# Kernel optimization log

Hardware: AMD Instinct MI355X
Metric: run time of the kernel (lower is better)

Reference implementation:

```python
import jax, jax.numpy as jnp
import numpy as np

L, S, N, E, H = 1024, 1024, 8, 1024, 16

def setup_inputs() -> dict:
    key = jax.random.key(0)
    k0, k1, k2, k3 = jax.random.split(key, 4)
    query = jax.random.normal(k0, (L, N, E), jnp.float32)
    key_t = jax.random.normal(k1, (S, N, E), jnp.float32)
    in_proj_weight = jax.random.normal(k2, (3 * E, E), jnp.float32) * (1.0 / np.sqrt(E))
    in_proj_bias = jnp.zeros((3 * E,), jnp.float32)
    attn_bias = jax.random.normal(k3, (N * H, L, S), jnp.float32) * 0.02
    return {"query": query, "key": key_t, "in_proj_weight": in_proj_weight,
            "in_proj_bias": in_proj_bias, "attn_bias": attn_bias}

def reference(query, key, in_proj_weight, in_proj_bias, attn_bias):
    tgt_len, bsz, embed_dim = query.shape
    head_dim = embed_dim // H
    scaling = float(head_dim) ** -0.5  # scale_factor = 1
    # q/k projections: first two embed_dim-row slices of in_proj_weight
    q = query @ in_proj_weight[:embed_dim].T + in_proj_bias[:embed_dim]
    k = key @ in_proj_weight[embed_dim:2 * embed_dim].T + in_proj_bias[embed_dim:2 * embed_dim]
    q = q * scaling
    # (L, N, E) -> (N*H, L, hd)
    q = q.reshape(tgt_len, bsz * H, head_dim).transpose(1, 0, 2)
    k = k.reshape(-1, bsz * H, head_dim).transpose(1, 0, 2)
    # scores: (N*H, L, S), additive bias, then stable softmax
    scores = jnp.einsum('bld,bsd->bls', q, k) + attn_bias
    attn_output_weights = jax.nn.softmax(scores, axis=-1)
    return attn_output_weights
```

## Files before the change

kernel.cpp:

```cpp
#include <hip/hip_runtime.h>
#include <hip/hip_bf16.h>
#include <stdint.h>

#define L_DIM 1024
#define S_DIM 1024
#define N_DIM 8
#define E_DIM 1024
#define H_DIM 16
#define HD    64
#define BH    (N_DIM*H_DIM)
#define M_ROWS (L_DIM*N_DIM)

typedef __bf16 bf16x8 __attribute__((ext_vector_type(8)));
typedef float  f32x4  __attribute__((ext_vector_type(4)));
typedef _Float16 f16;
typedef _Float16 f16x8 __attribute__((ext_vector_type(8)));
typedef unsigned short u16;
typedef unsigned short u16x8 __attribute__((ext_vector_type(8)));

__device__ inline u16 f2bf(float x){
  unsigned int u = __float_as_uint(x);
  u = (u + 0x7FFFu + ((u >> 16) & 1u)) >> 16;
  return (u16)u;
}

__global__ __launch_bounds__(256) void convert_kernel(
    const float* __restrict__ query, const float* __restrict__ key,
    const float* __restrict__ w,
    u16* __restrict__ qbf, u16* __restrict__ kbf,
    u16* __restrict__ wq, u16* __restrict__ wk)
{
  const int QN = M_ROWS*E_DIM;
  const int WN = E_DIM*E_DIM;
  const int total8 = (2*QN + 2*WN)/8;
  int stride = gridDim.x*blockDim.x;
  for (int g = blockIdx.x*blockDim.x + threadIdx.x; g < total8; g += stride) {
    int base = g*8;
    const float* src; u16* dst; float scale = 1.0f;
    if (base < QN)           { src = query + base;      dst = qbf + base; }
    else if (base < 2*QN)    { src = key + (base-QN);   dst = kbf + (base-QN); }
    else if (base < 2*QN+WN) { src = w + (base-2*QN);   dst = wq + (base-2*QN); scale = 0.125f; }
    else                     { src = w + (base-2*QN);   dst = wk + (base-2*QN-WN); }
    float4 v0 = *(const float4*)(src);
    float4 v1 = *(const float4*)(src+4);
    u16x8 o;
    o[0]=f2bf(v0.x*scale); o[1]=f2bf(v0.y*scale); o[2]=f2bf(v0.z*scale); o[3]=f2bf(v0.w*scale);
    o[4]=f2bf(v1.x*scale); o[5]=f2bf(v1.y*scale); o[6]=f2bf(v1.z*scale); o[7]=f2bf(v1.w*scale);
    *(u16x8*)dst = o;
  }
}

__global__ __launch_bounds__(256) void proj_gemm(
    const u16* __restrict__ A, const u16* __restrict__ W,
    const float* __restrict__ bias, float bscale,
    u16* __restrict__ C)
{
  __shared__ __align__(16) u16 As[128*32];
  __shared__ __align__(16) u16 Bs[128*32];
  const int t = threadIdx.x;
  const int lane = t & 63;
  const int w = t >> 6;
  const int wr = w >> 1, wc = w & 1;
  const int rowTile = blockIdx.x * 128;
  const int colTile = blockIdx.y * 128;

  f32x4 acc[4][4];
  #pragma unroll
  for (int m=0;m<4;m++)
    #pragma unroll
    for (int n=0;n<4;n++) acc[m][n] = (f32x4){0.f,0.f,0.f,0.f};

  uint32_t asBase = (uint32_t)(uintptr_t)&As[0];
  uint32_t bsBase = (uint32_t)(uintptr_t)&Bs[0];
  const char* Ab = (const char*)A;
  const char* Wb = (const char*)W;

  for (int kt = 0; kt < 32; ++kt) {
    __syncthreads();
    #pragma unroll
    for (int issue = 0; issue < 2; ++issue) {
      int o = issue*4096 + t*16;
      int row  = o >> 6;
      int colb = o & 63;
      const char* ga = Ab + (size_t)(rowTile + row)*2048 + kt*64 + colb;
      const char* gb = Wb + (size_t)(colTile + row)*2048 + kt*64 + colb;
      uint32_t la = asBase + issue*4096 + (w<<10);
      uint32_t lb = bsBase + issue*4096 + (w<<10);
      __builtin_amdgcn_global_load_lds(
          (const __attribute__((address_space(1))) void*)(uintptr_t)ga,
          (__attribute__((address_space(3))) void*)(uintptr_t)la, 16, 0, 0);
      __builtin_amdgcn_global_load_lds(
          (const __attribute__((address_space(1))) void*)(uintptr_t)gb,
          (__attribute__((address_space(3))) void*)(uintptr_t)lb, 16, 0, 0);
    }
    __syncthreads();

    bf16x8 af[4], bfr[4];
    int krow = (lane >> 4) * 16;
    #pragma unroll
    for (int m=0;m<4;m++) {
      int r = wr*64 + m*16 + (lane&15);
      af[m] = *(const bf16x8*)((const char*)As + r*64 + krow);
    }
    #pragma unroll
    for (int n=0;n<4;n++) {
      int r = wc*64 + n*16 + (lane&15);
      bfr[n] = *(const bf16x8*)((const char*)Bs + r*64 + krow);
    }
    #pragma unroll
    for (int m=0;m<4;m++)
      #pragma unroll
      for (int n=0;n<4;n++)
        acc[m][n] = __builtin_amdgcn_mfma_f32_16x16x32_bf16(af[m], bfr[n], acc[m][n], 0,0,0);
  }

  #pragma unroll
  for (int n=0;n<4;n++) {
    int gcol = colTile + wc*64 + n*16 + (lane&15);
    float bv = bias[gcol]*bscale;
    #pragma unroll
    for (int m=0;m<4;m++) {
      int grow0 = rowTile + wr*64 + m*16 + ((lane>>4)<<2);
      #pragma unroll
      for (int r=0;r<4;r++)
        C[(size_t)(grow0+r)*1024 + gcol] = f2bf(acc[m][n][r] + bv);
    }
  }
}

__global__ __launch_bounds__(256) void attn_softmax(
    const u16* __restrict__ Qb, const u16* __restrict__ Kb,
    const float* __restrict__ bias, float* __restrict__ out)
{
  __shared__ __align__(16) char scb[16*2048];
  const int t = threadIdx.x;
  const int lane = t & 63;
  const int w = t >> 6;
  const int ltile = blockIdx.x;
  const int b = blockIdx.y;
  const int n = b >> 4, h = b & 15;

  int l_row = ltile*16 + (lane & 15);
  size_t qoff = ((size_t)(l_row*8 + n))*1024 + h*64 + ((lane>>4)*8);
  bf16x8 a0 = *(const bf16x8*)(Qb + qoff);
  bf16x8 a1 = *(const bf16x8*)(Qb + qoff + 32);

  const int rowBase = (lane>>4)*4;

  for (int st = w; st < 64; st += 4) {
    int s_row = st*16 + (lane & 15);
    size_t koff = ((size_t)(s_row*8 + n))*1024 + h*64 + ((lane>>4)*8);
    bf16x8 b0 = *(const bf16x8*)(Kb + koff);
    bf16x8 b1 = *(const bf16x8*)(Kb + koff + 32);
    f32x4 acc = {0.f,0.f,0.f,0.f};
    acc = __builtin_amdgcn_mfma_f32_16x16x32_bf16(a0, b0, acc, 0,0,0);
    acc = __builtin_amdgcn_mfma_f32_16x16x32_bf16(a1, b1, acc, 0,0,0);
    int scol = st*16 + (lane & 15);
    #pragma unroll
    for (int r=0;r<4;r++) {
      int row = rowBase + r;
      int byte = (row*2048 + scol*2) ^ ((row&7)<<4);
      *(f16*)(scb + byte) = (f16)acc[r];
    }
  }
  __syncthreads();

  #pragma unroll
  for (int rr=0;rr<4;rr++) {
    int row = rr*4 + w;
    int l_glob = ltile*16 + row;
    const float* brow = bias + ((size_t)b*1024 + l_glob)*1024;
    float*       orow = out  + ((size_t)b*1024 + l_glob)*1024;
    const int swz = (row&7)<<4;
    float v[16];
    float mx = -1e30f;
    #pragma unroll
    for (int it=0; it<2; ++it) {
      int cb = it*1024 + lane*16;
      f16x8 s8 = *(const f16x8*)(scb + ((row*2048 + cb) ^ swz));
      int col = it*512 + lane*8;
      f32x4 b4a = __builtin_nontemporal_load((const f32x4*)(brow + col));
      f32x4 b4b = __builtin_nontemporal_load((const f32x4*)(brow + col + 4));
      #pragma unroll
      for (int j=0;j<4;j++) v[it*8+j]   = (float)s8[j]   + b4a[j];
      #pragma unroll
      for (int j=0;j<4;j++) v[it*8+4+j] = (float)s8[4+j] + b4b[j];
    }
    #pragma unroll
    for (int j=0;j<16;j++) mx = fmaxf(mx, v[j]);
    #pragma unroll
    for (int off=32; off>0; off>>=1) mx = fmaxf(mx, __shfl_xor(mx, off, 64));
    float sum = 0.f;
    #pragma unroll
    for (int j=0;j<16;j++) { v[j] = __expf(v[j]-mx); sum += v[j]; }
    #pragma unroll
    for (int off=32; off>0; off>>=1) sum += __shfl_xor(sum, off, 64);
    float inv = 1.0f / sum;
    #pragma unroll
    for (int it=0; it<2; ++it) {
      int col = it*512 + lane*8;
      f32x4 o4a = { v[it*8+0]*inv, v[it*8+1]*inv, v[it*8+2]*inv, v[it*8+3]*inv };
      f32x4 o4b = { v[it*8+4]*inv, v[it*8+5]*inv, v[it*8+6]*inv, v[it*8+7]*inv };
      __builtin_nontemporal_store(o4a, (f32x4*)(orow + col));
      __builtin_nontemporal_store(o4b, (f32x4*)(orow + col + 4));
    }
  }
}

extern "C" void kernel_launch(void* const* d_in, const int* in_sizes, int n_in,
                              void* d_out, int out_size, void* d_ws, size_t ws_size,
                              hipStream_t stream) {
  const float* query = (const float*)d_in[0];
  const float* key   = (const float*)d_in[1];
  const float* w     = (const float*)d_in[2];
  const float* bias  = (const float*)d_in[3];
  const float* abias = (const float*)d_in[4];
  float* out = (float*)d_out;

  char* ws = (char*)d_ws;
  const size_t QKB = (size_t)M_ROWS*E_DIM*2;
  const size_t WB  = (size_t)E_DIM*E_DIM*2;
  u16* qbf = (u16*)ws;  ws += QKB;
  u16* kbf = (u16*)ws;  ws += QKB;
  u16* wq  = (u16*)ws;  ws += WB;
  u16* wk  = (u16*)ws;  ws += WB;
  u16* Qp  = (u16*)ws;  ws += QKB;
  u16* Kp  = (u16*)ws;  ws += QKB;

  hipLaunchKernelGGL(convert_kernel, dim3(2048), dim3(256), 0, stream,
                     query, key, w, qbf, kbf, wq, wk);
  hipLaunchKernelGGL(proj_gemm, dim3(64, 8), dim3(256), 0, stream,
                     qbf, wq, bias, 0.125f, Qp);
  hipLaunchKernelGGL(proj_gemm, dim3(64, 8), dim3(256), 0, stream,
                     kbf, wk, bias + 1024, 1.0f, Kp);
  hipLaunchKernelGGL(attn_softmax, dim3(64, 128), dim3(256), 0, stream,
                     Qp, Kp, abias, out);
}
```

Baseline: 386.5 us.

## Store projected Q/K head-major and stage K tiles through swizzled LDS

```diff
diff --git a/kernel.cpp b/kernel.cpp
--- a/kernel.cpp
+++ b/kernel.cpp
@@ -10,6 +10,9 @@
 #define HD    64
 #define BH    (N_DIM*H_DIM)
 #define M_ROWS (L_DIM*N_DIM)
+
+#define AS1 __attribute__((address_space(1)))
+#define AS3 __attribute__((address_space(3)))
 
 typedef __bf16 bf16x8 __attribute__((ext_vector_type(8)));
 typedef float  f32x4  __attribute__((ext_vector_type(4)));
@@ -87,11 +90,9 @@
       uint32_t la = asBase + issue*4096 + (w<<10);
       uint32_t lb = bsBase + issue*4096 + (w<<10);
       __builtin_amdgcn_global_load_lds(
-          (const __attribute__((address_space(1))) void*)(uintptr_t)ga,
-          (__attribute__((address_space(3))) void*)(uintptr_t)la, 16, 0, 0);
+          (const AS1 void*)(uintptr_t)ga, (AS3 void*)(uintptr_t)la, 16, 0, 0);
       __builtin_amdgcn_global_load_lds(
-          (const __attribute__((address_space(1))) void*)(uintptr_t)gb,
-          (__attribute__((address_space(3))) void*)(uintptr_t)lb, 16, 0, 0);
+          (const AS1 void*)(uintptr_t)gb, (AS3 void*)(uintptr_t)lb, 16, 0, 0);
     }
     __syncthreads();
 
@@ -115,52 +116,72 @@
   }
 
   #pragma unroll
-  for (int n=0;n<4;n++) {
-    int gcol = colTile + wc*64 + n*16 + (lane&15);
+  for (int n2=0;n2<4;n2++) {
+    int gcol = colTile + wc*64 + n2*16 + (lane&15);
+    int h = gcol >> 6, d = gcol & 63;
     float bv = bias[gcol]*bscale;
     #pragma unroll
     for (int m=0;m<4;m++) {
       int grow0 = rowTile + wr*64 + m*16 + ((lane>>4)<<2);
       #pragma unroll
-      for (int r=0;r<4;r++)
-        C[(size_t)(grow0+r)*1024 + gcol] = f2bf(acc[m][n][r] + bv);
+      for (int r=0;r<4;r++) {
+        int grow = grow0 + r;
+        int l = grow >> 3, nn = grow & 7;
+        C[((size_t)(nn*16 + h)*1024 + l)*64 + d] = f2bf(acc[m][n2][r] + bv);
+      }
     }
   }
 }
 
 __global__ __launch_bounds__(256) void attn_softmax(
-    const u16* __restrict__ Qb, const u16* __restrict__ Kb,
+    const u16* __restrict__ Qh, const u16* __restrict__ Kh,
     const float* __restrict__ bias, float* __restrict__ out)
 {
   __shared__ __align__(16) char scb[16*2048];
+  __shared__ __align__(16) char kbuf[8192];
   const int t = threadIdx.x;
   const int lane = t & 63;
   const int w = t >> 6;
   const int ltile = blockIdx.x;
   const int b = blockIdx.y;
-  const int n = b >> 4, h = b & 15;
-
-  int l_row = ltile*16 + (lane & 15);
-  size_t qoff = ((size_t)(l_row*8 + n))*1024 + h*64 + ((lane>>4)*8);
+
+  const char* Kb = (const char*)(Kh + (size_t)b*1024*64);
+  const u16*  Qb = Qh + (size_t)b*1024*64 + (size_t)ltile*16*64;
+
+  int qoff = (lane&15)*64 + (lane>>4)*8;
   bf16x8 a0 = *(const bf16x8*)(Qb + qoff);
   bf16x8 a1 = *(const bf16x8*)(Qb + qoff + 32);
 
   const int rowBase = (lane>>4)*4;
-
-  for (int st = w; st < 64; st += 4) {
-    int s_row = st*16 + (lane & 15);
-    size_t koff = ((size_t)(s_row*8 + n))*1024 + h*64 + ((lane>>4)*8);
-    bf16x8 b0 = *(const bf16x8*)(Kb + koff);
-    bf16x8 b1 = *(const bf16x8*)(Kb + koff + 32);
+  uint32_t kbase = (uint32_t)(uintptr_t)&kbuf[0];
+
+  for (int g = 0; g < 16; ++g) {
+    __syncthreads();
+    #pragma unroll
+    for (int rd = 0; rd < 2; ++rd) {
+      int o = rd*4096 + t*16;
+      int src = o ^ (((o>>7)&7)<<4);
+      __builtin_amdgcn_global_load_lds(
+          (const AS1 void*)(uintptr_t)(Kb + (size_t)g*8192 + src),
+          (AS3 void*)(uintptr_t)(kbase + rd*4096 + (w<<10)), 16, 0, 0);
+    }
+    __syncthreads();
+
+    int r = w*16 + (lane&15);
+    int byte0 = r*128 + ((lane>>4)*16);
+    int swzk = (r&7)<<4;
+    bf16x8 b0 = *(const bf16x8*)(kbuf + ((byte0      ) ^ swzk));
+    bf16x8 b1 = *(const bf16x8*)(kbuf + ((byte0 + 64 ) ^ swzk));
     f32x4 acc = {0.f,0.f,0.f,0.f};
     acc = __builtin_amdgcn_mfma_f32_16x16x32_bf16(a0, b0, acc, 0,0,0);
     acc = __builtin_amdgcn_mfma_f32_16x16x32_bf16(a1, b1, acc, 0,0,0);
-    int scol = st*16 + (lane & 15);
-    #pragma unroll
-    for (int r=0;r<4;r++) {
-      int row = rowBase + r;
+
+    int scol = g*64 + w*16 + (lane & 15);
+    #pragma unroll
+    for (int rr=0;rr<4;rr++) {
+      int row = rowBase + rr;
       int byte = (row*2048 + scol*2) ^ ((row&7)<<4);
-      *(f16*)(scb + byte) = (f16)acc[r];
+      *(f16*)(scb + byte) = (f16)acc[rr];
     }
   }
   __syncthreads();
@@ -179,8 +200,8 @@
       int cb = it*1024 + lane*16;
       f16x8 s8 = *(const f16x8*)(scb + ((row*2048 + cb) ^ swz));
       int col = it*512 + lane*8;
-      f32x4 b4a = __builtin_nontemporal_load((const f32x4*)(brow + col));
-      f32x4 b4b = __builtin_nontemporal_load((const f32x4*)(brow + col + 4));
+      f32x4 b4a = *(const f32x4*)(brow + col);
+      f32x4 b4b = *(const f32x4*)(brow + col + 4);
       #pragma unroll
       for (int j=0;j<4;j++) v[it*8+j]   = (float)s8[j]   + b4a[j];
       #pragma unroll
@@ -201,8 +222,8 @@
       int col = it*512 + lane*8;
       f32x4 o4a = { v[it*8+0]*inv, v[it*8+1]*inv, v[it*8+2]*inv, v[it*8+3]*inv };
       f32x4 o4b = { v[it*8+4]*inv, v[it*8+5]*inv, v[it*8+6]*inv, v[it*8+7]*inv };
-      __builtin_nontemporal_store(o4a, (f32x4*)(orow + col));
-      __builtin_nontemporal_store(o4b, (f32x4*)(orow + col + 4));
+      *(f32x4*)(orow + col)     = o4a;
+      *(f32x4*)(orow + col + 4) = o4b;
     }
   }
 }
@@ -224,15 +245,15 @@
   u16* kbf = (u16*)ws;  ws += QKB;
   u16* wq  = (u16*)ws;  ws += WB;
   u16* wk  = (u16*)ws;  ws += WB;
-  u16* Qp  = (u16*)ws;  ws += QKB;
-  u16* Kp  = (u16*)ws;  ws += QKB;
+  u16* Qh  = (u16*)ws;  ws += QKB;
+  u16* Kh  = (u16*)ws;  ws += QKB;
 
   hipLaunchKernelGGL(convert_kernel, dim3(2048), dim3(256), 0, stream,
                      query, key, w, qbf, kbf, wq, wk);
   hipLaunchKernelGGL(proj_gemm, dim3(64, 8), dim3(256), 0, stream,
-                     qbf, wq, bias, 0.125f, Qp);
+                     qbf, wq, bias, 0.125f, Qh);
   hipLaunchKernelGGL(proj_gemm, dim3(64, 8), dim3(256), 0, stream,
-                     kbf, wk, bias + 1024, 1.0f, Kp);
+                     kbf, wk, bias + 1024, 1.0f, Kh);
   hipLaunchKernelGGL(attn_softmax, dim3(64, 128), dim3(256), 0, stream,
-                     Qp, Kp, abias, out);
-}
+                     Qh, Kh, abias, out);
+}
```

Result: faster. 322.3 us (-16.6%).
